# Optimization experiments

Hardware: AMD Instinct MI355X
Metric: run time of the kernel (lower is better)

Reference implementation:

```python
import jax, jax.numpy as jnp
import numpy as np

TAU = 0.07          # softmax temperature
THR = 0.3           # Jaccard similarity threshold for positive pairs
EPS_NORM = 1e-12    # F.normalize eps


def setup_inputs() -> dict:
    key = jax.random.key(0)
    k1, k2, k3 = jax.random.split(key, 3)
    N, D, A = 4096, 128, 512
    z1 = jax.random.normal(k1, (N, D), dtype=jnp.float32)
    z2 = jax.random.normal(k2, (N, D), dtype=jnp.float32)
    labels = jax.random.randint(k3, (N, A), 0, 2).astype(jnp.int32)
    return {"z1": z1, "z2": z2, "labels": labels}


def _l2_normalize(x):
    n = jnp.linalg.norm(x, axis=-1, keepdims=True)
    return x / jnp.maximum(n, EPS_NORM)


def reference(z1, z2, labels):
    # Implements the N > 1000 (chunked) branch of SupConLoss.forward,
    # vectorized over all anchors at once (chunking is just tiling; math identical).
    N = z1.shape[0]
    idx = jnp.arange(N)

    z1n = _l2_normalize(z1)                       # (N, D)
    z2n = _l2_normalize(z2)                       # (N, D)
    z_all = jnp.concatenate([z1n, z2n], axis=0)   # (2N, D)

    # Jaccard label similarity -> positive-pair mask
    lab = labels.astype(jnp.float32)              # (N, A)
    inter = lab @ lab.T                           # (N, N)
    s = lab.sum(axis=1, keepdims=True)            # (N, 1)
    union = s + s.T - inter
    jaccard = inter / (union + 1e-8)
    pos_label = jaccard >= THR                    # (N, N) bool

    # pos mask over 2N columns: label-positives in both halves,
    # augmented view [j, N+j] forced True, self column [j, j] forced False.
    pos_mask = jnp.concatenate([pos_label, pos_label], axis=1)  # (N, 2N)
    pos_mask = pos_mask.at[idx, N + idx].set(True)
    pos_mask = pos_mask.at[idx, idx].set(False)

    # similarity of z1 anchors against all 2N embeddings
    sim = (z1n @ z_all.T) / TAU                   # (N, 2N)
    sim = sim - jax.lax.stop_gradient(sim.max(axis=1, keepdims=True))
    exp_sim = jnp.exp(sim)

    # denominator excludes the self column [j, j]
    denom = exp_sim.sum(axis=1, keepdims=True) - exp_sim[idx, idx][:, None]
    log_prob = sim - jnp.log(denom + 1e-8)

    num_pos = jnp.maximum(pos_mask.sum(axis=1), 1)
    loss_per_sample = -jnp.where(pos_mask, log_prob, 0.0).sum(axis=1) / num_pos
    return loss_per_sample.sum() / N
```

## Files before the change

kernel.cpp:

```cpp
#include <hip/hip_runtime.h>
#include <math.h>

#define N_ROWS 4096
#define DIM    128
#define A_LAB  512
#define INV_TAU 14.285714285714286f
#define C_EXP   20.609929155556620f

typedef __attribute__((ext_vector_type(8))) short short8;
typedef __attribute__((ext_vector_type(4))) float f32x4;
typedef __attribute__((ext_vector_type(4))) int i32x4;
typedef __attribute__((ext_vector_type(16))) int i32x16;


__device__ __forceinline__ unsigned short f2bf(float f) {
  unsigned int u = __builtin_bit_cast(unsigned int, f);
  u += 0x7fffu + ((u >> 16) & 1u);
  return (unsigned short)(u >> 16);
}

__global__ __launch_bounds__(256) void k_norm_pack(
    const float* __restrict__ z1, const float* __restrict__ z2,
    const int* __restrict__ labels,
    unsigned int* __restrict__ zbf, uint2* __restrict__ labs8,
    int* __restrict__ s, float* __restrict__ part, float* __restrict__ out)
{
  {
    const int idx = blockIdx.x * 256 + threadIdx.x;
    if (idx < 3 * 4096) part[idx] = 0.0f;
    if (idx == 0) out[0] = 0.0f;
  }
  const int wave = threadIdx.x >> 6, lane = threadIdx.x & 63;
  const int r = blockIdx.x * 4 + wave;
  const float* src = (r < N_ROWS) ? (z1 + (size_t)r * DIM)
                                  : (z2 + (size_t)(r - N_ROWS) * DIM);
  float2 x = ((const float2*)src)[lane];
  float ss = x.x * x.x + x.y * x.y;
  #pragma unroll
  for (int off = 32; off > 0; off >>= 1) ss += __shfl_xor(ss, off);
  const float inv = 1.0f / fmaxf(sqrtf(ss), 1e-12f);
  const unsigned int lo = f2bf(x.x * inv);
  const unsigned int hi = f2bf(x.y * inv);
  {
    const int u = lane >> 2, p = lane & 3;
    const int kf = u >> 2, quad = u & 3;
    const int g = r >> 4;
    zbf[(size_t)(((g * 4 + kf) * 64) + ((r & 15) + (quad << 4))) * 4 + p] = (hi << 16) | lo;
  }

  if (r < N_ROWS) {
    const int4* lp = (const int4*)(labels + (size_t)r * A_LAB);
    const int4 a = lp[2 * lane], b = lp[2 * lane + 1];
    const unsigned int w0 = (unsigned int)(a.x != 0)       | ((unsigned int)(a.y != 0) << 8)
                          | ((unsigned int)(a.z != 0) << 16) | ((unsigned int)(a.w != 0) << 24);
    const unsigned int w1 = (unsigned int)(b.x != 0)       | ((unsigned int)(b.y != 0) << 8)
                          | ((unsigned int)(b.z != 0) << 16) | ((unsigned int)(b.w != 0) << 24);
    uint2 v; v.x = w0; v.y = w1;
    const int ul = lane >> 1, hp = lane & 1;
    const int ks = ul >> 1, h = ul & 1;
    const int g = r >> 5;
    labs8[(size_t)(((g * 16 + ks) * 64) + ((r & 31) + (h << 5))) * 2 + hp] = v;
    int cnt = __popc(w0) + __popc(w1);
    #pragma unroll
    for (int off = 32; off > 0; off >>= 1) cnt += __shfl_xor(cnt, off);
    if (lane == 0) s[r] = cnt;
  }
}

__global__ __launch_bounds__(512, 4) void k_fused(
    const unsigned char* __restrict__ labs8, const int* __restrict__ s,
    const unsigned short* __restrict__ zbf, float* __restrict__ part)
{
  __shared__ unsigned int pmL[128 * 4];
  __shared__ __align__(16) char bpanel[32768];
  const int tid = threadIdx.x;
  const int ibase = blockIdx.x * 128, jbase = blockIdx.y * 128;
  const int wave = tid >> 6, lane = tid & 63;
  const bool diag = (ibase == jbase);
  const char* gl = (const char*)labs8;
  const char* gz = (const char*)zbf;

  const int jwr = (wave >> 2) * 64;
  const int jwc = (wave & 3) * 32;
  const int col32 = lane & 31, h = lane >> 5;

  const int s3i = 3 * s[ibase + jwr + lane];
  const int s3j = 3 * s[jbase + jwc + col32];

  i32x16 jacc[2];
  #pragma unroll
  for (int rt = 0; rt < 2; ++rt)
    #pragma unroll
    for (int e = 0; e < 16; ++e) jacc[rt][e] = 0;

  const int gI = (ibase + jwr) >> 5;
  const int gJ = (jbase + jwc) >> 5;
  #pragma unroll
  for (int ks = 0; ks < 16; ++ks) {
    i32x4 a[2], b;
    #pragma unroll
    for (int rt = 0; rt < 2; ++rt)
      a[rt] = *(const i32x4*)(gl + (size_t)(((gI + rt) * 16 + ks) * 64 + lane) * 16);
    b = *(const i32x4*)(gl + (size_t)((gJ * 16 + ks) * 64 + lane) * 16);
    #pragma unroll
    for (int rt = 0; rt < 2; ++rt)
      jacc[rt] = __builtin_amdgcn_mfma_i32_32x32x32_i8(a[rt], b, jacc[rt], 0, 0, 0);
  }

  const int wl = wave & 3;
  #pragma unroll
  for (int rt = 0; rt < 2; ++rt)
    #pragma unroll
    for (int reg = 0; reg < 16; ++reg) {
      const int r0 = (reg & 3) + 8 * (reg >> 2);
      const int si = __shfl(s3i, rt * 32 + r0 + 4 * h);
      const bool pred = 13 * jacc[rt][reg] >= si + s3j;
      const unsigned long long bal = __ballot(pred);
      const int lr = jwr + rt * 32 + r0;
      if (lane == 0)      pmL[lr * 4 + wl]       = (unsigned int)bal;
      else if (lane == 1) pmL[(lr + 4) * 4 + wl] = (unsigned int)(bal >> 32);
    }

  const int col = lane & 15, quad = lane >> 4;
  const int srow = wave * 16;
  const int gA = (ibase + srow) >> 4;
  short8 afr[4];
  #pragma unroll
  for (int kf = 0; kf < 4; ++kf)
    afr[kf] = *(const short8*)(gz + (size_t)((gA * 4 + kf) * 64 + lane) * 16);

  {
    const char* srcp = gz + (size_t)(jbase >> 4) * 4096;
    #pragma unroll
    for (int q = 0; q < 4; ++q)
      *(uint4*)(bpanel + (size_t)(q * 512 + tid) * 16) =
          *(const uint4*)(srcp + (size_t)(q * 512 + tid) * 16);
  }

  __syncthreads();

  uint4 pw[4];
  #pragma unroll
  for (int reg = 0; reg < 4; ++reg)
    pw[reg] = *(const uint4*)&pmL[(srow + quad * 4 + reg) * 4];

  float lacc[4], Sacc[4], Pcnt[4];
  #pragma unroll
  for (int reg = 0; reg < 4; ++reg) { lacc[reg] = 0; Sacc[reg] = 0; Pcnt[reg] = 0; }

  #pragma unroll
  for (int half = 0; half < 2; ++half) {
    if (half == 1) {
      __syncthreads();
      const char* srcp = gz + (size_t)((N_ROWS + jbase) >> 4) * 4096;
      #pragma unroll
      for (int q = 0; q < 4; ++q)
        *(uint4*)(bpanel + (size_t)(q * 512 + tid) * 16) =
            *(const uint4*)(srcp + (size_t)(q * 512 + tid) * 16);
      __syncthreads();
    }

    f32x4 acc[8];
    #pragma unroll
    for (int nt = 0; nt < 8; ++nt) acc[nt] = (f32x4){0, 0, 0, 0};

    #pragma unroll
    for (int nt = 0; nt < 8; ++nt) {
      short8 bfr[4];
      #pragma unroll
      for (int kf = 0; kf < 4; ++kf)
        bfr[kf] = *(const short8*)(bpanel + (size_t)((nt * 4 + kf) * 64 + lane) * 16);
      #pragma unroll
      for (int kf = 0; kf < 4; ++kf)
        acc[nt] = __builtin_amdgcn_mfma_f32_16x16x32_bf16(afr[kf], bfr[kf], acc[nt], 0, 0, 0);
    }

    if (!diag) {
      #pragma unroll
      for (int nt = 0; nt < 8; ++nt) {
        const int bitpos = (nt & 1) * 16 + col;
        #pragma unroll
        for (int reg = 0; reg < 4; ++reg) {
          const unsigned int w = ((const unsigned int*)&pw[reg])[nt >> 1];
          const float d = acc[nt][reg];
          lacc[reg] += exp2f(fmaf(d, C_EXP, -C_EXP));
          if ((w >> bitpos) & 1) Sacc[reg] += d;
        }
      }
    } else {
      const bool left = (half == 0);
      #pragma unroll
      for (int nt = 0; nt < 8; ++nt) {
        const int joff = nt * 16 + col;
        const int jc = jbase + joff;
        const int bitpos = joff & 31;
        #pragma unroll
        for (int reg = 0; reg < 4; ++reg) {
          const int i = ibase + srow + quad * 4 + reg;
          const unsigned int w = ((const unsigned int*)&pw[reg])[nt >> 1];
          const float d = acc[nt][reg];
          const bool bit = (w >> bitpos) & 1;
          const bool self = left && (jc == i);
          const bool pos = left ? (bit && !self) : (bit || (jc == i));
          const float e = exp2f(fmaf(d, C_EXP, -C_EXP));
          if (!self) lacc[reg] += e;
          if (pos) { Sacc[reg] += d; Pcnt[reg] += 1.0f; }
        }
      }
    }
  }

  #pragma unroll
  for (int reg = 0; reg < 4; ++reg) {
    float l = lacc[reg], S = Sacc[reg], P = Pcnt[reg];
    #pragma unroll
    for (int m = 1; m < 16; m <<= 1) {
      l += __shfl_xor(l, m);
      S += __shfl_xor(S, m);
      if (diag) P += __shfl_xor(P, m);
    }
    if (col == 0) {
      const int li = srow + quad * 4 + reg;
      const int i = ibase + li;
      if (!diag) {
        const uint4 w = pw[reg];
        P = 2.0f * (float)(__popc(w.x) + __popc(w.y) + __popc(w.z) + __popc(w.w));
      }
      atomicAdd(&part[i], l);
      atomicAdd(&part[4096 + i], S);
      atomicAdd(&part[8192 + i], P);
    }
  }
}

__global__ __launch_bounds__(128) void k_loss(
    const float* __restrict__ part, float* __restrict__ out)
{
  const int a = blockIdx.x * 128 + threadIdx.x;
  const float l = part[a];
  const float S = part[4096 + a];
  const float P = part[8192 + a];
  const float np = fmaxf(P, 1.0f);
  float v = INV_TAU + logf(l + 1e-8f) - (S * INV_TAU) / np;
  #pragma unroll
  for (int off = 32; off > 0; off >>= 1) v += __shfl_xor(v, off);
  __shared__ float ws2[2];
  const int wave = threadIdx.x >> 6, lane = threadIdx.x & 63;
  if (lane == 0) ws2[wave] = v;
  __syncthreads();
  if (threadIdx.x == 0) atomicAdd(out, (ws2[0] + ws2[1]) * (1.0f / (float)N_ROWS));
}

extern "C" void kernel_launch(void* const* d_in, const int* in_sizes, int n_in,
                              void* d_out, int out_size, void* d_ws, size_t ws_size,
                              hipStream_t stream) {
  const float* z1 = (const float*)d_in[0];
  const float* z2 = (const float*)d_in[1];
  const int* labels = (const int*)d_in[2];
  float* out = (float*)d_out;
  char* ws = (char*)d_ws;

  unsigned int* zbf    = (unsigned int*)(ws);
  uint2* labs8         = (uint2*)(ws + 2097152);
  int* s               = (int*)(ws + 4194304);
  float* part          = (float*)(ws + 4210688);

  hipLaunchKernelGGL(k_norm_pack, dim3(2048), dim3(256), 0, stream,
                     z1, z2, labels, zbf, labs8, s, part, out);
  hipLaunchKernelGGL(k_fused, dim3(32, 32), dim3(512), 0, stream,
                     (const unsigned char*)labs8, s, (const unsigned short*)zbf, part);
  hipLaunchKernelGGL(k_loss, dim3(32), dim3(128), 0, stream, part, out);
}
```

Measured before the change: 104.3 us.

## Split Jaccard mask into symmetric upper-triangle kernel writing a global bitmask

Moves the int8 MFMA Jaccard computation out of the fused similarity kernel into a separate kernel. That kernel covers only the 528 upper-triangular 128x128 tiles and writes both the tile mask and its transpose into a global bit matrix. The fused kernel then reads the positive-mask words from global memory instead of computing them. This halves the label-intersection MFMA work by exploiting symmetry, at the cost of an extra launch, a 2 MB bitmask round trip, and scattered transposed writes.

```diff
diff --git a/kernel.cpp b/kernel.cpp
--- a/kernel.cpp
+++ b/kernel.cpp
@@ -67,18 +67,19 @@
   }
 }
 
-__global__ __launch_bounds__(512, 4) void k_fused(
+__global__ __launch_bounds__(512, 4) void k_jac(
     const unsigned char* __restrict__ labs8, const int* __restrict__ s,
-    const unsigned short* __restrict__ zbf, float* __restrict__ part)
+    unsigned int* __restrict__ pm)
 {
-  __shared__ unsigned int pmL[128 * 4];
-  __shared__ __align__(16) char bpanel[32768];
+  int r = blockIdx.x, row = 0;
+  while (r >= 32 - row) { r -= 32 - row; ++row; }
+  const int bi = row, bj = row + r;
+  const int ibase = bi * 128, jbase = bj * 128;
+  const bool diag = (bi == bj);
+
   const int tid = threadIdx.x;
-  const int ibase = blockIdx.x * 128, jbase = blockIdx.y * 128;
   const int wave = tid >> 6, lane = tid & 63;
-  const bool diag = (ibase == jbase);
   const char* gl = (const char*)labs8;
-  const char* gz = (const char*)zbf;
 
   const int jwr = (wave >> 2) * 64;
   const int jwc = (wave & 3) * 32;
@@ -108,6 +109,8 @@
   }
 
   const int wl = wave & 3;
+  const int jw0 = (jbase >> 5);
+  unsigned int tw0 = 0, tw1 = 0;
   #pragma unroll
   for (int rt = 0; rt < 2; ++rt)
     #pragma unroll
@@ -117,13 +120,40 @@
       const bool pred = 13 * jacc[rt][reg] >= si + s3j;
       const unsigned long long bal = __ballot(pred);
       const int lr = jwr + rt * 32 + r0;
-      if (lane == 0)      pmL[lr * 4 + wl]       = (unsigned int)bal;
-      else if (lane == 1) pmL[(lr + 4) * 4 + wl] = (unsigned int)(bal >> 32);
-    }
+      if (lane == 0)      pm[(size_t)(ibase + lr) * 128 + jw0 + wl]       = (unsigned int)bal;
+      else if (lane == 1) pm[(size_t)(ibase + lr + 4) * 128 + jw0 + wl]   = (unsigned int)(bal >> 32);
+      const unsigned int pb = ((unsigned int)pred) << (r0 + 4 * h);
+      if (rt == 0) tw0 |= pb; else tw1 |= pb;
+    }
+  if (!diag) {
+    tw0 |= __shfl_xor(tw0, 32);
+    tw1 |= __shfl_xor(tw1, 32);
+    const size_t trow = (size_t)(jbase + jwc + col32) * 128 + (ibase >> 5) + (jwr >> 5);
+    if (h == 0) pm[trow]     = tw0;
+    else        pm[trow + 1] = tw1;
+  }
+}
+
+__global__ __launch_bounds__(512, 4) void k_fused(
+    const unsigned int* __restrict__ pm,
+    const unsigned short* __restrict__ zbf, float* __restrict__ part)
+{
+  __shared__ __align__(16) char bpanel[32768];
+  const int tid = threadIdx.x;
+  const int ibase = blockIdx.x * 128, jbase = blockIdx.y * 128;
+  const int wave = tid >> 6, lane = tid & 63;
+  const bool diag = (ibase == jbase);
+  const char* gz = (const char*)zbf;
 
   const int col = lane & 15, quad = lane >> 4;
   const int srow = wave * 16;
   const int gA = (ibase + srow) >> 4;
+
+  uint4 pw[4];
+  #pragma unroll
+  for (int reg = 0; reg < 4; ++reg)
+    pw[reg] = *(const uint4*)&pm[(size_t)(ibase + srow + quad * 4 + reg) * 128 + (jbase >> 5)];
+
   short8 afr[4];
   #pragma unroll
   for (int kf = 0; kf < 4; ++kf)
@@ -138,11 +168,6 @@
   }
 
   __syncthreads();
-
-  uint4 pw[4];
-  #pragma unroll
-  for (int reg = 0; reg < 4; ++reg)
-    pw[reg] = *(const uint4*)&pmL[(srow + quad * 4 + reg) * 4];
 
   float lacc[4], Sacc[4], Pcnt[4];
   #pragma unroll
@@ -220,8 +245,7 @@
       if (diag) P += __shfl_xor(P, m);
     }
     if (col == 0) {
-      const int li = srow + quad * 4 + reg;
-      const int i = ibase + li;
+      const int i = ibase + srow + quad * 4 + reg;
       if (!diag) {
         const uint4 w = pw[reg];
         P = 2.0f * (float)(__popc(w.x) + __popc(w.y) + __popc(w.z) + __popc(w.w));
@@ -264,10 +288,13 @@
   uint2* labs8         = (uint2*)(ws + 2097152);
   int* s               = (int*)(ws + 4194304);
   float* part          = (float*)(ws + 4210688);
+  unsigned int* pm     = (unsigned int*)(ws + 4259840);
 
   hipLaunchKernelGGL(k_norm_pack, dim3(2048), dim3(256), 0, stream,
                      z1, z2, labels, zbf, labs8, s, part, out);
+  hipLaunchKernelGGL(k_jac, dim3(528), dim3(512), 0, stream,
+                     (const unsigned char*)labs8, s, pm);
   hipLaunchKernelGGL(k_fused, dim3(32, 32), dim3(512), 0, stream,
-                     (const unsigned char*)labs8, s, (const unsigned short*)zbf, part);
+                     pm, (const unsigned short*)zbf, part);
   hipLaunchKernelGGL(k_loss, dim3(32), dim3(128), 0, stream, part, out);
 }
```

Result: no change. 105.6 us (+1.2%).

## Compute Jaccard mask with bit-packed popcount in separate kernel

Applied to the files above, without the earlier changes.

Replaces the int8 MFMA label-intersection inside the fused kernel with a bitpacked label format (512 bits per row) and a dedicated kernel that computes intersections via AND+popcount, writing a global bitmask. The fused similarity kernel then just loads the precomputed mask words. This cuts label data volume 8x and removes the int8 MFMA work and its LDS ballot staging from the fused kernel. In exchange it adds a kernel launch, a global round trip for the 2 MB mask, and a heavy scalar popcount loop (16 popcounts per pair) on VALU.

```diff
diff --git a/kernel.cpp b/kernel.cpp
--- a/kernel.cpp
+++ b/kernel.cpp
@@ -9,8 +9,6 @@
 
 typedef __attribute__((ext_vector_type(8))) short short8;
 typedef __attribute__((ext_vector_type(4))) float f32x4;
-typedef __attribute__((ext_vector_type(4))) int i32x4;
-typedef __attribute__((ext_vector_type(16))) int i32x16;
 
 
 __device__ __forceinline__ unsigned short f2bf(float f) {
@@ -22,7 +20,7 @@
 __global__ __launch_bounds__(256) void k_norm_pack(
     const float* __restrict__ z1, const float* __restrict__ z2,
     const int* __restrict__ labels,
-    unsigned int* __restrict__ zbf, uint2* __restrict__ labs8,
+    unsigned int* __restrict__ zbf, unsigned char* __restrict__ plab,
     int* __restrict__ s, float* __restrict__ part, float* __restrict__ out)
 {
   {
@@ -51,79 +49,95 @@
   if (r < N_ROWS) {
     const int4* lp = (const int4*)(labels + (size_t)r * A_LAB);
     const int4 a = lp[2 * lane], b = lp[2 * lane + 1];
-    const unsigned int w0 = (unsigned int)(a.x != 0)       | ((unsigned int)(a.y != 0) << 8)
-                          | ((unsigned int)(a.z != 0) << 16) | ((unsigned int)(a.w != 0) << 24);
-    const unsigned int w1 = (unsigned int)(b.x != 0)       | ((unsigned int)(b.y != 0) << 8)
-                          | ((unsigned int)(b.z != 0) << 16) | ((unsigned int)(b.w != 0) << 24);
-    uint2 v; v.x = w0; v.y = w1;
-    const int ul = lane >> 1, hp = lane & 1;
-    const int ks = ul >> 1, h = ul & 1;
-    const int g = r >> 5;
-    labs8[(size_t)(((g * 16 + ks) * 64) + ((r & 31) + (h << 5))) * 2 + hp] = v;
-    int cnt = __popc(w0) + __popc(w1);
+    const unsigned int p8 =
+        (unsigned int)(a.x != 0)        | ((unsigned int)(a.y != 0) << 1)
+      | ((unsigned int)(a.z != 0) << 2) | ((unsigned int)(a.w != 0) << 3)
+      | ((unsigned int)(b.x != 0) << 4) | ((unsigned int)(b.y != 0) << 5)
+      | ((unsigned int)(b.z != 0) << 6) | ((unsigned int)(b.w != 0) << 7);
+    plab[(size_t)r * 64 + lane] = (unsigned char)p8;
+    int cnt = __popc(p8);
     #pragma unroll
     for (int off = 32; off > 0; off >>= 1) cnt += __shfl_xor(cnt, off);
     if (lane == 0) s[r] = cnt;
   }
 }
 
+__global__ __launch_bounds__(256, 2) void k_jac(
+    const uint4* __restrict__ plab4, const int* __restrict__ s,
+    unsigned int* __restrict__ pm)
+{
+  __shared__ __align__(16) uint4 cpan[128 * 4];
+  __shared__ int cs[128];
+
+  const int tid = threadIdx.x;
+  const int j0 = blockIdx.x * 128;
+  const int i  = blockIdx.y * 256 + tid;
+
+  cpan[tid]       = plab4[(size_t)(j0 + (tid >> 2)) * 4 + (tid & 3)];
+  cpan[256 + tid] = plab4[(size_t)(j0 + 64 + (tid >> 2)) * 4 + (tid & 3)];
+  if (tid < 128) cs[tid] = 3 * s[j0 + tid];
+
+  uint4 rw0 = plab4[(size_t)i * 4 + 0];
+  uint4 rw1 = plab4[(size_t)i * 4 + 1];
+  uint4 rw2 = plab4[(size_t)i * 4 + 2];
+  uint4 rw3 = plab4[(size_t)i * 4 + 3];
+  const int s3i = 3 * s[i];
+
+  __syncthreads();
+
+  #pragma unroll 1
+  for (int wq = 0; wq < 4; ++wq) {
+    unsigned int mw = 0;
+    #pragma unroll 8
+    for (int jj = 0; jj < 32; ++jj) {
+      const int jl = wq * 32 + jj;
+      const uint4 c0 = cpan[jl * 4 + 0];
+      const uint4 c1 = cpan[jl * 4 + 1];
+      const uint4 c2 = cpan[jl * 4 + 2];
+      const uint4 c3 = cpan[jl * 4 + 3];
+      int inter = __popc(rw0.x & c0.x);
+      inter += __popc(rw0.y & c0.y);
+      inter += __popc(rw0.z & c0.z);
+      inter += __popc(rw0.w & c0.w);
+      inter += __popc(rw1.x & c1.x);
+      inter += __popc(rw1.y & c1.y);
+      inter += __popc(rw1.z & c1.z);
+      inter += __popc(rw1.w & c1.w);
+      inter += __popc(rw2.x & c2.x);
+      inter += __popc(rw2.y & c2.y);
+      inter += __popc(rw2.z & c2.z);
+      inter += __popc(rw2.w & c2.w);
+      inter += __popc(rw3.x & c3.x);
+      inter += __popc(rw3.y & c3.y);
+      inter += __popc(rw3.z & c3.z);
+      inter += __popc(rw3.w & c3.w);
+      const bool ok = 13 * inter >= s3i + cs[jl];
+      mw |= ((unsigned int)ok) << jj;
+    }
+    pm[(size_t)i * 128 + blockIdx.x * 4 + wq] = mw;
+  }
+}
+
 __global__ __launch_bounds__(512, 4) void k_fused(
-    const unsigned char* __restrict__ labs8, const int* __restrict__ s,
+    const unsigned int* __restrict__ pm,
     const unsigned short* __restrict__ zbf, float* __restrict__ part)
 {
-  __shared__ unsigned int pmL[128 * 4];
   __shared__ __align__(16) char bpanel[32768];
   const int tid = threadIdx.x;
   const int ibase = blockIdx.x * 128, jbase = blockIdx.y * 128;
   const int wave = tid >> 6, lane = tid & 63;
   const bool diag = (ibase == jbase);
-  const char* gl = (const char*)labs8;
   const char* gz = (const char*)zbf;
-
-  const int jwr = (wave >> 2) * 64;
-  const int jwc = (wave & 3) * 32;
-  const int col32 = lane & 31, h = lane >> 5;
-
-  const int s3i = 3 * s[ibase + jwr + lane];
-  const int s3j = 3 * s[jbase + jwc + col32];
-
-  i32x16 jacc[2];
-  #pragma unroll
-  for (int rt = 0; rt < 2; ++rt)
-    #pragma unroll
-    for (int e = 0; e < 16; ++e) jacc[rt][e] = 0;
-
-  const int gI = (ibase + jwr) >> 5;
-  const int gJ = (jbase + jwc) >> 5;
-  #pragma unroll
-  for (int ks = 0; ks < 16; ++ks) {
-    i32x4 a[2], b;
-    #pragma unroll
-    for (int rt = 0; rt < 2; ++rt)
-      a[rt] = *(const i32x4*)(gl + (size_t)(((gI + rt) * 16 + ks) * 64 + lane) * 16);
-    b = *(const i32x4*)(gl + (size_t)((gJ * 16 + ks) * 64 + lane) * 16);
-    #pragma unroll
-    for (int rt = 0; rt < 2; ++rt)
-      jacc[rt] = __builtin_amdgcn_mfma_i32_32x32x32_i8(a[rt], b, jacc[rt], 0, 0, 0);
-  }
-
-  const int wl = wave & 3;
-  #pragma unroll
-  for (int rt = 0; rt < 2; ++rt)
-    #pragma unroll
-    for (int reg = 0; reg < 16; ++reg) {
-      const int r0 = (reg & 3) + 8 * (reg >> 2);
-      const int si = __shfl(s3i, rt * 32 + r0 + 4 * h);
-      const bool pred = 13 * jacc[rt][reg] >= si + s3j;
-      const unsigned long long bal = __ballot(pred);
-      const int lr = jwr + rt * 32 + r0;
-      if (lane == 0)      pmL[lr * 4 + wl]       = (unsigned int)bal;
-      else if (lane == 1) pmL[(lr + 4) * 4 + wl] = (unsigned int)(bal >> 32);
-    }
 
   const int col = lane & 15, quad = lane >> 4;
   const int srow = wave * 16;
   const int gA = (ibase + srow) >> 4;
+
+  uint4 pw[4];
+  #pragma unroll
+  for (int reg = 0; reg < 4; ++reg)
+    pw[reg] = *(const uint4*)&pm[(size_t)(ibase + srow + quad * 4 + reg) * 128 + (jbase >> 5)];
+
   short8 afr[4];
   #pragma unroll
   for (int kf = 0; kf < 4; ++kf)
@@ -138,11 +152,6 @@
   }
 
   __syncthreads();
-
-  uint4 pw[4];
-  #pragma unroll
-  for (int reg = 0; reg < 4; ++reg)
-    pw[reg] = *(const uint4*)&pmL[(srow + quad * 4 + reg) * 4];
 
   float lacc[4], Sacc[4], Pcnt[4];
   #pragma unroll
@@ -220,8 +229,7 @@
       if (diag) P += __shfl_xor(P, m);
     }
     if (col == 0) {
-      const int li = srow + quad * 4 + reg;
-      const int i = ibase + li;
+      const int i = ibase + srow + quad * 4 + reg;
       if (!diag) {
         const uint4 w = pw[reg];
         P = 2.0f * (float)(__popc(w.x) + __popc(w.y) + __popc(w.z) + __popc(w.w));
@@ -261,13 +269,16 @@
   char* ws = (char*)d_ws;
 
   unsigned int* zbf    = (unsigned int*)(ws);
-  uint2* labs8         = (uint2*)(ws + 2097152);
+  unsigned char* plab  = (unsigned char*)(ws + 2097152);
   int* s               = (int*)(ws + 4194304);
   float* part          = (float*)(ws + 4210688);
+  unsigned int* pm     = (unsigned int*)(ws + 4259840);
 
   hipLaunchKernelGGL(k_norm_pack, dim3(2048), dim3(256), 0, stream,
-                     z1, z2, labels, zbf, labs8, s, part, out);
+                     z1, z2, labels, zbf, plab, s, part, out);
+  hipLaunchKernelGGL(k_jac, dim3(32, 16), dim3(256), 0, stream,
+                     (const uint4*)plab, s, pm);
   hipLaunchKernelGGL(k_fused, dim3(32, 32), dim3(512), 0, stream,
-                     (const unsigned char*)labs8, s, (const unsigned short*)zbf, part);
+                     pm, (const unsigned short*)zbf, part);
   hipLaunchKernelGGL(k_loss, dim3(32), dim3(128), 0, stream, part, out);
 }
```

New measurement: 117.5 us. 1.13x slower.
